# Kernel tuning notes

Hardware: AMD Instinct MI355X
Metric: run time of the kernel (lower is better)

## Reference

```python
import jax, jax.numpy as jnp
import numpy as np

D_MODEL = 512
D_ALPHA = 100
D_PH = 80
SCALE = 1.0 / np.sqrt(D_MODEL)


def gru_cell(x, h, Wih, Whh, bih, bhh):
    # PyTorch GRU gate order: r, z, n
    gi = x @ Wih.T + bih
    gh = h @ Whh.T + bhh
    ir, iz, inn = jnp.split(gi, 3, axis=-1)
    hr, hz, hn = jnp.split(gh, 3, axis=-1)
    r = jax.nn.sigmoid(ir + hr)
    z = jax.nn.sigmoid(iz + hz)
    n = jnp.tanh(inn + r * hn)
    return (1.0 - z) * n + z * h


def attend(q, k, v):
    # q: [B,D], k/v: [B,L,D]
    scores = jnp.einsum('bd,bld->bl', q, k) * SCALE
    a = jax.nn.softmax(scores, axis=-1)  # [B,L]
    o = jnp.einsum('bl,bld->bd', a, v)
    return a, o


def setup_inputs() -> dict:
    key = jax.random.key(0)
    ks = jax.random.split(key, 25)
    D = D_MODEL

    def u(k, shape, fan):
        return jax.random.uniform(k, shape, jnp.float32, -1.0, 1.0) / np.sqrt(fan)

    inp = {
        'text': jax.random.randint(ks[0], (256, 128), 0, D_ALPHA),
        'tgt': jax.random.randint(ks[1], (256, 64), 0, D_PH),
        'E_alpha': jax.random.normal(ks[2], (D_ALPHA, D), jnp.float32),
        'enc_Wih_f': u(ks[3], (3 * D, D), D),
        'enc_Whh_f': u(ks[4], (3 * D, D), D),
        'enc_bih_f': u(ks[5], (3 * D,), D),
        'enc_bhh_f': u(ks[6], (3 * D,), D),
        'enc_Wih_b': u(ks[7], (3 * D, D), D),
        'enc_Whh_b': u(ks[8], (3 * D, D), D),
        'enc_bih_b': u(ks[9], (3 * D,), D),
        'enc_bhh_b': u(ks[10], (3 * D,), D),
        'hpost_W': u(ks[11], (D, 2 * D), 2 * D),
        'hpost_b': u(ks[12], (D,), 2 * D),
        'wk_W': u(ks[13], (D, 2 * D), 2 * D),
        'wk_b': u(ks[14], (D,), 2 * D),
        'wv_W': u(ks[15], (D, 2 * D), 2 * D),
        'wv_b': u(ks[16], (D,), 2 * D),
        'E_ph': jax.random.normal(ks[17], (D_PH, D), jnp.float32),
        'dec_Wih': u(ks[18], (3 * D, 2 * D), 2 * D),
        'dec_Whh': u(ks[19], (3 * D, D), D),
        'dec_bih': u(ks[20], (3 * D,), D),
        'dec_bhh': u(ks[21], (3 * D,), D),
        'post_W': u(ks[22], (D_PH, D), D),
        'post_b': u(ks[23], (D_PH,), D),
    }
    return inp


def reference(text, tgt, E_alpha, enc_Wih_f, enc_Whh_f, enc_bih_f, enc_bhh_f,
              enc_Wih_b, enc_Whh_b, enc_bih_b, enc_bhh_b, hpost_W, hpost_b,
              wk_W, wk_b, wv_W, wv_b, E_ph, dec_Wih, dec_Whh, dec_bih,
              dec_bhh, post_W, post_b):
    B, LT = text.shape
    LP = tgt.shape[1]

    # ---- Encoder: bidirectional single-layer GRU (eval: dropout = identity)
    emb = E_alpha[text]                     # [B,LT,D]
    xs = jnp.swapaxes(emb, 0, 1)            # [LT,B,D]
    h0 = jnp.zeros((B, D_MODEL), emb.dtype)

    def mk_step(Wih, Whh, bih, bhh):
        def step(h, x):
            h2 = gru_cell(x, h, Wih, Whh, bih, bhh)
            return h2, h2
        return step

    hF, ysF = jax.lax.scan(mk_step(enc_Wih_f, enc_Whh_f, enc_bih_f, enc_bhh_f), h0, xs)
    hB, ysB = jax.lax.scan(mk_step(enc_Wih_b, enc_Whh_b, enc_bih_b, enc_bhh_b), h0, xs[::-1])
    ysB = ysB[::-1]
    enc_o = jnp.swapaxes(jnp.concatenate([ysF, ysB], axis=-1), 0, 1)  # [B,LT,2D]
    h = jnp.tanh(jnp.concatenate([hF, hB], axis=-1) @ hpost_W.T + hpost_b)  # [B,D]

    k = enc_o @ wk_W.T + wk_b               # [B,LT,D]
    v = enc_o @ wv_W.T + wv_b               # [B,LT,D]

    # ---- initial attention from encoder hidden; eval-mode first token is argmax
    # over tgt[:,0] reshaped to [B,1,1], i.e. always index 0.
    a_sl0, a_o0 = attend(h, k, v)
    dec_i0 = jnp.zeros((B,), jnp.int32)

    def dstep(carry, _):
        hh, a_o, a_sl, dec_i = carry
        e = E_ph[dec_i]                                  # [B,D]
        x = gru_cell(jnp.concatenate([e, a_o], axis=-1), hh,
                     dec_Wih, dec_Whh, dec_bih, dec_bhh)  # [B,D]
        o = x @ post_W.T + post_b                         # [B,D_PH]
        n_sl, n_o = attend(x, k, v)
        nxt = jnp.argmax(o, axis=-1).astype(jnp.int32)
        return (x, n_o, n_sl, nxt), (a_sl, o)

    _, (attn_t, res_t) = jax.lax.scan(dstep, (h, a_o0, a_sl0, dec_i0), None, length=LP)
    attn = jnp.swapaxes(attn_t, 0, 1)        # [B,LP,LT]
    res = jnp.swapaxes(res_t, 0, 1)          # [B,LP,D_PH]
    return attn, res
```

## Files before the change

kernel.cpp:

```cpp
#include <hip/hip_runtime.h>
#include <math.h>

#define B   256
#define LT  128
#define LP  64
#define DM  512
#define D3  1536
#define DPH 80
#define SCALE_F 0.044194173824159216f

__device__ __forceinline__ float dot4(float4 a, float4 b) {
    return a.x*b.x + a.y*b.y + a.z*b.z + a.w*b.w;
}
__device__ __forceinline__ float sigmoidf_(float x) {
    return 1.0f / (1.0f + expf(-x));
}

__device__ __forceinline__ float4 issue_bypass4(const float* p) {
    float4 v;
    asm volatile("global_load_dwordx4 %0, %1, off sc0 sc1"
                 : "=v"(v) : "v"(p));
    return v;
}
__device__ __forceinline__ void wait_vm0() {
    asm volatile("s_waitcnt vmcnt(0)" ::: "memory");
    __builtin_amdgcn_sched_barrier(0);
}

__device__ __forceinline__ void group_barrier(int* cnt, int target) {
    __syncthreads();
    if (threadIdx.x == 0) {
        __hip_atomic_fetch_add(cnt, 1, __ATOMIC_RELEASE,
                               __HIP_MEMORY_SCOPE_AGENT);
        while (__hip_atomic_load(cnt, __ATOMIC_RELAXED,
                                 __HIP_MEMORY_SCOPE_AGENT) < target)
            __builtin_amdgcn_s_sleep(16);
    }
    __syncthreads();
}

__global__ __launch_bounds__(256) void precompG_kernel(
    const float* __restrict__ Emb, const float* __restrict__ W,
    const float* __restrict__ bias, float* __restrict__ G,
    int wstride, int woff)
{
    const int n  = blockIdx.x * 256 + threadIdx.x;
    const int r0 = blockIdx.y * 4;
    __shared__ float es[4][DM];
    for (int i = threadIdx.x; i < 4 * DM; i += 256)
        es[i >> 9][i & 511] = Emb[(r0 + (i >> 9)) * DM + (i & 511)];
    __syncthreads();
    float acc[4] = {0.f, 0.f, 0.f, 0.f};
    const float* wr = &W[(size_t)n * wstride + woff];
    for (int j = 0; j < DM; j += 4) {
        float4 w4 = *(const float4*)&wr[j];
        #pragma unroll
        for (int rr = 0; rr < 4; ++rr) {
            float4 e4 = *(const float4*)&es[rr][j];
            acc[rr] += dot4(e4, w4);
        }
    }
    float bv = bias[n];
    #pragma unroll
    for (int rr = 0; rr < 4; ++rr)
        G[(r0 + rr) * D3 + n] = acc[rr] + bv;
}

__global__ __launch_bounds__(512, 1) void enc_persist_kernel(
    const float* __restrict__ Gf, const float* __restrict__ Gb,
    const float* __restrict__ Whh_f, const float* __restrict__ Whh_b,
    const float* __restrict__ bhh_f, const float* __restrict__ bhh_b,
    const int* __restrict__ text,
    float* __restrict__ hF0, float* __restrict__ hF1,
    float* __restrict__ hB0, float* __restrict__ hB1,
    float* __restrict__ E,
    const float* __restrict__ hpost_W, const float* __restrict__ hpost_b,
    float* __restrict__ hd0, int* __restrict__ bar)
{
    __shared__ float Wl[48][516];
    __shared__ float As[2][64][36];
    __shared__ float xs[1024];
    __shared__ float bl[48];

    const int tid  = threadIdx.x;
    const int blk  = blockIdx.x;
    const int dir  = blk & 1;
    const int bblk = (blk >> 1) & 3;
    const int jblk = blk >> 3;
    const int jtile = jblk * 16;
    const int btile = bblk * 64;
    int* cnt = bar + (blk & 7);

    const float* G   = dir ? Gb : Gf;
    const float* Whh = dir ? Whh_b : Whh_f;
    const float* bhh = dir ? bhh_b : bhh_f;
    float* h0 = dir ? hB0 : hF0;
    float* h1 = dir ? hB1 : hF1;
    const int yoff = dir ? DM : 0;

    for (int i = tid; i < 48 * 128; i += 512) {
        const int r = i >> 7, c = (i & 127) << 2;
        *(float4*)&Wl[r][c] =
            *(const float4*)&Whh[(size_t)((r >> 4) * DM + jtile + (r & 15)) * DM + c];
    }
    if (tid < 48) bl[tid] = bhh[(tid >> 4) * DM + jtile + (tid & 15)];
    __syncthreads();

    const int jj   = tid & 15;
    const int rg   = tid >> 4;
    const int lrow = tid >> 3;
    const int lcol = (tid & 7) * 4;

    for (int s = 0; s < LT; ++s) {
        const int t = dir ? (LT - 1 - s) : s;
        const float* hin = (s & 1) ? h1 : h0;
        float* hout      = (s & 1) ? h0 : h1;

        float acc[2][3];
        #pragma unroll
        for (int m = 0; m < 2; ++m) {
            acc[m][0] = 0.f; acc[m][1] = 0.f; acc[m][2] = 0.f;
        }

        float4 rA = issue_bypass4(&hin[(btile + lrow) * DM + lcol]);
        wait_vm0();
        int buf = 0;
        for (int kc = 0; kc < 16; ++kc) {
            *(float4*)&As[buf][lrow][lcol] = rA;
            __syncthreads();
            float4 nA;
            if (kc < 15)
                nA = issue_bypass4(&hin[(btile + lrow) * DM + (kc + 1) * 32 + lcol]);
            const int kb = kc * 32;
            #pragma unroll
            for (int c4 = 0; c4 < 8; ++c4) {
                float4 bv0 = *(float4*)&Wl[jj][kb + c4 * 4];
                float4 bv1 = *(float4*)&Wl[16 + jj][kb + c4 * 4];
                float4 bv2 = *(float4*)&Wl[32 + jj][kb + c4 * 4];
                #pragma unroll
                for (int m = 0; m < 2; ++m) {
                    float4 av = *(float4*)&As[buf][rg * 2 + m][c4 * 4];
                    acc[m][0] += dot4(av, bv0);
                    acc[m][1] += dot4(av, bv1);
                    acc[m][2] += dot4(av, bv2);
                }
            }
            if (kc < 15) { wait_vm0(); rA = nA; }
            buf ^= 1;
        }

        const int j = jtile + jj;
        #pragma unroll
        for (int m = 0; m < 2; ++m) {
            const int b = btile + rg * 2 + m;
            const int c = text[b * LT + t];
            float hr = acc[m][0] + bl[jj];
            float hz = acc[m][1] + bl[16 + jj];
            float hn = acc[m][2] + bl[32 + jj];
            float r = sigmoidf_(G[c * D3 + j] + hr);
            float z = sigmoidf_(G[c * D3 + DM + j] + hz);
            float n = tanhf(G[c * D3 + 2 * DM + j] + r * hn);
            float hp = hin[b * DM + j];
            float hv = (1.f - z) * n + z * hp;
            hout[b * DM + j] = hv;
            E[(size_t)(b * LT + t) * 1024 + yoff + j] = hv;
        }
        if (s < LT - 1) group_barrier(cnt, 32 * (s + 1));
    }

    group_barrier(bar + 8, 256);
    {
        const int b = blk;
        if (tid < 256) {
            float4 v = issue_bypass4((tid < 128)
                ? &hF0[b * DM + tid * 4]
                : &hB0[b * DM + (tid - 128) * 4]);
            wait_vm0();
            *(float4*)&xs[tid * 4] = v;
        }
        __syncthreads();
        if (tid < DM) {
            const float* wr = &hpost_W[tid * 1024];
            float acc = 0.f;
            for (int jx = 0; jx < 1024; jx += 4)
                acc += dot4(*(const float4*)&xs[jx], *(const float4*)&wr[jx]);
            hd0[b * DM + tid] = tanhf(acc + hpost_b[tid]);
        }
    }
}

__global__ __launch_bounds__(256) void kv_chunk_kernel(
    const float* __restrict__ E,
    const float* __restrict__ wk, const float* __restrict__ wv,
    const float* __restrict__ kb, const float* __restrict__ vb,
    float* __restrict__ T, int r0)
{
    __shared__ float As[64][36];
    __shared__ float Bk[64][36];
    __shared__ float Bv[64][36];
    const int tid = threadIdx.x;
    const int nn = tid & 15, bb = tid >> 4;
    const int ntile = blockIdx.x * 64;
    const int mtile = blockIdx.y * 64;

    float ak[4][4], av_[4][4];
    #pragma unroll
    for (int m = 0; m < 4; ++m)
        #pragma unroll
        for (int i = 0; i < 4; ++i) { ak[m][i] = 0.f; av_[m][i] = 0.f; }

    const int lrow = tid >> 3;
    const int lcol = (tid & 7) * 4;

    for (int k0 = 0; k0 < 1024; k0 += 32) {
        __syncthreads();
        *(float4*)&As[lrow][lcol] =
            *(const float4*)&E[(size_t)(r0 + mtile + lrow) * 1024 + k0 + lcol];
        *(float4*)&As[lrow + 32][lcol] =
            *(const float4*)&E[(size_t)(r0 + mtile + lrow + 32) * 1024 + k0 + lcol];
        *(float4*)&Bk[lrow][lcol] =
            *(const float4*)&wk[(ntile + lrow) * 1024 + k0 + lcol];
        *(float4*)&Bk[lrow + 32][lcol] =
            *(const float4*)&wk[(ntile + lrow + 32) * 1024 + k0 + lcol];
        *(float4*)&Bv[lrow][lcol] =
            *(const float4*)&wv[(ntile + lrow) * 1024 + k0 + lcol];
        *(float4*)&Bv[lrow + 32][lcol] =
            *(const float4*)&wv[(ntile + lrow + 32) * 1024 + k0 + lcol];
        __syncthreads();
        #pragma unroll
        for (int c4 = 0; c4 < 8; ++c4) {
            float4 a4[4], k4[4], v4[4];
            #pragma unroll
            for (int m = 0; m < 4; ++m) a4[m] = *(float4*)&As[bb + 16 * m][c4 * 4];
            #pragma unroll
            for (int i = 0; i < 4; ++i) {
                k4[i] = *(float4*)&Bk[nn + 16 * i][c4 * 4];
                v4[i] = *(float4*)&Bv[nn + 16 * i][c4 * 4];
            }
            #pragma unroll
            for (int m = 0; m < 4; ++m)
                #pragma unroll
                for (int i = 0; i < 4; ++i) {
                    ak[m][i]  += dot4(a4[m], k4[i]);
                    av_[m][i] += dot4(a4[m], v4[i]);
                }
        }
    }
    #pragma unroll
    for (int m = 0; m < 4; ++m) {
        const int lm = mtile + bb + 16 * m;
        #pragma unroll
        for (int i = 0; i < 4; ++i) {
            const int gn = ntile + nn + 16 * i;
            T[(size_t)lm * 1024 + gn]       = ak[m][i]  + kb[gn];
            T[(size_t)lm * 1024 + DM + gn]  = av_[m][i] + vb[gn];
        }
    }
}

__global__ __launch_bounds__(256) void copy4_kernel(
    float4* __restrict__ dst, const float4* __restrict__ src, int n4)
{
    int i = blockIdx.x * 256 + threadIdx.x;
    const int stride = gridDim.x * 256;
    for (; i < n4; i += stride) dst[i] = src[i];
}

__device__ __forceinline__ void attend_body(
    int b, int tid, const float* __restrict__ q, const float* __restrict__ EKV,
    const float* __restrict__ post_W, const float* __restrict__ post_b,
    float* __restrict__ attn, float* __restrict__ res,
    float* __restrict__ a_o, int* __restrict__ dec_i,
    int s, int attn_row, int do_post, int do_attn,
    float* qs, float* part, float* sarr, float* red, float4 (*pvp)[128])
{
    if (tid < 128) {
        float4 qv = issue_bypass4(&q[b * DM + tid * 4]);
        wait_vm0();
        *(float4*)&qs[tid * 4] = qv;
    }
    __syncthreads();

    if (do_post) {
        if (tid < DPH) {
            const float* wr = &post_W[tid * DM];
            float acc = 0.f;
            for (int d = 0; d < DM; d += 4)
                acc += dot4(*(const float4*)&qs[d], *(const float4*)&wr[d]);
            float lv = acc + post_b[tid];
            res[(size_t)(b * LP + s) * DPH + tid] = lv;
            part[tid] = lv;
        }
        __syncthreads();
        if (tid == 0) {
            float best = part[0]; int bi = 0;
            for (int p = 1; p < DPH; ++p) {
                float vv = part[p];
                if (vv > best) { best = vv; bi = p; }
            }
            dec_i[b] = bi;
        }
        __syncthreads();
    }

    if (do_attn) {
        {
            const int r = tid & 127, quad = tid >> 7;
            const float* kr = &EKV[(size_t)(b * LT + r) * 1024 + quad * 128];
            const float* qh = &qs[quad * 128];
            float p0 = 0.f, p1 = 0.f;
            #pragma unroll
            for (int d = 0; d < 128; d += 8) {
                p0 += dot4(*(const float4*)&qh[d],     *(const float4*)&kr[d]);
                p1 += dot4(*(const float4*)&qh[d + 4], *(const float4*)&kr[d + 4]);
            }
            part[tid] = p0 + p1;
        }
        __syncthreads();
        if (tid < LT)
            sarr[tid] = (((part[tid] + part[tid + 128]) + part[tid + 256])
                         + part[tid + 384]) * SCALE_F;
        __syncthreads();
        if (tid < 64) {
            float m = fmaxf(sarr[tid], sarr[tid + 64]);
            #pragma unroll
            for (int off = 32; off > 0; off >>= 1)
                m = fmaxf(m, __shfl_xor(m, off));
            if (tid == 0) red[0] = m;
        }
        __syncthreads();
        const float smax = red[0];
        if (tid < LT) sarr[tid] = expf(sarr[tid] - smax);
        __syncthreads();
        if (tid < 64) {
            float ssum = sarr[tid] + sarr[tid + 64];
            #pragma unroll
            for (int off = 32; off > 0; off >>= 1)
                ssum += __shfl_xor(ssum, off);
            if (tid == 0) red[1] = ssum;
        }
        __syncthreads();
        const float inv = 1.0f / red[1];
        if (tid < LT) {
            float a = sarr[tid] * inv;
            sarr[tid] = a;
            attn[(size_t)(b * LP + attn_row) * LT + tid] = a;
        }
        __syncthreads();
        {
            const int d4 = tid & 127, quad = tid >> 7;
            const float* vb0 = &EKV[(size_t)b * LT * 1024 + DM];
            float4 a0 = make_float4(0.f, 0.f, 0.f, 0.f);
            float4 a1 = make_float4(0.f, 0.f, 0.f, 0.f);
            const int l0 = quad * 32;
            #pragma unroll
            for (int l = l0; l < l0 + 32; l += 2) {
                float w0 = sarr[l], w1 = sarr[l + 1];
                float4 v0 = *(const float4*)&vb0[(size_t)l * 1024 + d4 * 4];
                float4 v1 = *(const float4*)&vb0[(size_t)(l + 1) * 1024 + d4 * 4];
                a0.x += w0 * v0.x; a0.y += w0 * v0.y;
                a0.z += w0 * v0.z; a0.w += w0 * v0.w;
                a1.x += w1 * v1.x; a1.y += w1 * v1.y;
                a1.z += w1 * v1.z; a1.w += w1 * v1.w;
            }
            pvp[quad][d4] = make_float4(a0.x + a1.x, a0.y + a1.y,
                                        a0.z + a1.z, a0.w + a1.w);
        }
        __syncthreads();
        if (tid < 128) {
            float4 p0 = pvp[0][tid], p1 = pvp[1][tid];
            float4 p2 = pvp[2][tid], p3 = pvp[3][tid];
            float4 o = make_float4(((p0.x + p1.x) + p2.x) + p3.x,
                                   ((p0.y + p1.y) + p2.y) + p3.y,
                                   ((p0.z + p1.z) + p2.z) + p3.z,
                                   ((p0.w + p1.w) + p2.w) + p3.w);
            *(float4*)&a_o[b * DM + tid * 4] = o;
        }
    }
}

__global__ __launch_bounds__(512, 1) void dec_persist_kernel(
    const float* __restrict__ Gd,
    const float* __restrict__ dec_Wih, const float* __restrict__ dec_Whh,
    const float* __restrict__ dec_bhh,
    const float* __restrict__ EKV,
    const float* __restrict__ post_W, const float* __restrict__ post_b,
    float* __restrict__ attn, float* __restrict__ res,
    float* __restrict__ a_o, int* __restrict__ dec_i,
    float* __restrict__ hd0, float* __restrict__ hd1,
    int* __restrict__ bar)
{
    __shared__ float Wi[24][516];
    __shared__ float Wh[24][516];
    __shared__ float As[2][64][36];
    __shared__ float bl[24];
    __shared__ float qs[DM];
    __shared__ float part[512];
    __shared__ float sarr[LT];
    __shared__ float red[2];
    __shared__ float4 pvp[4][128];

    const int tid  = threadIdx.x;
    const int blk  = blockIdx.x;
    const int bblk = blk & 3;
    const int jblk = blk >> 2;
    const int jtile = jblk * 8;
    const int btile = bblk * 64;
    const int arow  = btile + jblk;
    int* cnt = bar + 9 + bblk;
    int nb = 0;

    for (int i = tid; i < 24 * 128; i += 512) {
        const int r = i >> 7, c = (i & 127) << 2;
        const int wrow = (r >> 3) * DM + jtile + (r & 7);
        *(float4*)&Wi[r][c] =
            *(const float4*)&dec_Wih[(size_t)wrow * 1024 + DM + c];
        *(float4*)&Wh[r][c] =
            *(const float4*)&dec_Whh[(size_t)wrow * DM + c];
    }
    if (tid < 24) bl[tid] = dec_bhh[(tid >> 3) * DM + jtile + (tid & 7)];
    __syncthreads();

    attend_body(arow, tid, hd0, EKV, post_W, post_b, attn, res, a_o, dec_i,
                0, 0, 0, 1, qs, part, sarr, red, pvp);
    ++nb; group_barrier(cnt, 64 * nb);

    const int jj   = tid & 7;
    const int rr   = tid >> 3;
    const int lrow = tid >> 3;
    const int lcol = (tid & 7) * 4;

    for (int s = 0; s < LP; ++s) {
        const float* hin = (s & 1) ? hd1 : hd0;
        float* hout      = (s & 1) ? hd0 : hd1;

        float acc[4] = {0.f, 0.f, 0.f, 0.f};

        #pragma unroll
        for (int ph = 0; ph < 2; ++ph) {
            const float* Aptr = (ph == 0) ? a_o : hin;
            const float (*W)[516] = (ph == 0) ? Wi : Wh;

            float4 rA = issue_bypass4(&Aptr[(btile + lrow) * DM + lcol]);
            wait_vm0();
            int buf = (ph == 0) ? 0 : 0;
            for (int kc = 0; kc < 16; ++kc) {
                *(float4*)&As[buf][lrow][lcol] = rA;
                __syncthreads();
                float4 nA;
                if (kc < 15)
                    nA = issue_bypass4(&Aptr[(btile + lrow) * DM + (kc + 1) * 32 + lcol]);
                const int kb = kc * 32;
                #pragma unroll
                for (int c4 = 0; c4 < 8; ++c4) {
                    float4 bv0 = *(float4*)&W[jj][kb + c4 * 4];
                    float4 bv1 = *(float4*)&W[8 + jj][kb + c4 * 4];
                    float4 bv2 = *(float4*)&W[16 + jj][kb + c4 * 4];
                    float4 av  = *(float4*)&As[buf][rr][c4 * 4];
                    acc[0]      += dot4(av, bv0);
                    acc[1]      += dot4(av, bv1);
                    acc[2 + ph] += dot4(av, bv2);
                }
                if (kc < 15) { wait_vm0(); rA = nA; }
                buf ^= 1;
            }
            __syncthreads();
        }

        {
            const int j = jtile + jj;
            const int b = btile + rr;
            const int c = __hip_atomic_load(&dec_i[b], __ATOMIC_RELAXED,
                                            __HIP_MEMORY_SCOPE_SYSTEM);
            float r = sigmoidf_(Gd[c * D3 + j] + bl[jj] + acc[0]);
            float z = sigmoidf_(Gd[c * D3 + DM + j] + bl[8 + jj] + acc[1]);
            float n = tanhf(Gd[c * D3 + 2 * DM + j] + acc[2]
                            + r * (acc[3] + bl[16 + jj]));
            float hp = hin[b * DM + j];
            hout[b * DM + j] = (1.f - z) * n + z * hp;
        }
        ++nb; group_barrier(cnt, 64 * nb);

        attend_body(arow, tid, hout, EKV, post_W, post_b, attn, res, a_o, dec_i,
                    s, s + 1, 1, (s < LP - 1) ? 1 : 0,
                    qs, part, sarr, red, pvp);
        if (s < LP - 1) { ++nb; group_barrier(cnt, 64 * nb); }
    }
}

extern "C" void kernel_launch(void* const* d_in, const int* in_sizes, int n_in,
                              void* d_out, int out_size, void* d_ws, size_t ws_size,
                              hipStream_t stream)
{
    const int*   text    = (const int*)d_in[0];
    const float* E_alpha = (const float*)d_in[2];
    const float* Wih_f   = (const float*)d_in[3];
    const float* Whh_f   = (const float*)d_in[4];
    const float* bih_f   = (const float*)d_in[5];
    const float* bhh_f   = (const float*)d_in[6];
    const float* Wih_b   = (const float*)d_in[7];
    const float* Whh_b   = (const float*)d_in[8];
    const float* bih_b   = (const float*)d_in[9];
    const float* bhh_b   = (const float*)d_in[10];
    const float* hpost_W = (const float*)d_in[11];
    const float* hpost_b = (const float*)d_in[12];
    const float* wk_W    = (const float*)d_in[13];
    const float* wk_b    = (const float*)d_in[14];
    const float* wv_W    = (const float*)d_in[15];
    const float* wv_b    = (const float*)d_in[16];
    const float* E_ph    = (const float*)d_in[17];
    const float* dec_Wih = (const float*)d_in[18];
    const float* dec_Whh = (const float*)d_in[19];
    const float* dec_bih = (const float*)d_in[20];
    const float* dec_bhh = (const float*)d_in[21];
    const float* post_W  = (const float*)d_in[22];
    const float* post_b  = (const float*)d_in[23];

    float* ws = (float*)d_ws;
    float* Gf  = ws;
    float* Gb  = Gf  + 153600;
    float* Gd  = Gb  + 153600;
    float* hF0 = Gd  + 122880;
    float* hF1 = hF0 + 131072;
    float* hB0 = hF1 + 131072;
    float* hB1 = hB0 + 131072;
    float* hd0 = hB1 + 131072;
    float* hd1 = hd0 + 131072;
    float* a_o = hd1 + 131072;
    int*   dec_i = (int*)(a_o + 131072);
    int*   bar   = dec_i + 256;
    float* E   = a_o + 131072 + 512;
    float* T   = E + 33554432;

    hipMemsetAsync(hF0, 0, 131072 * sizeof(float), stream);
    hipMemsetAsync(hB0, 0, 131072 * sizeof(float), stream);
    hipMemsetAsync(dec_i, 0, (256 + 16) * sizeof(int), stream);

    precompG_kernel<<<dim3(6, 25), 256, 0, stream>>>(E_alpha, Wih_f, bih_f, Gf, DM, 0);
    precompG_kernel<<<dim3(6, 25), 256, 0, stream>>>(E_alpha, Wih_b, bih_b, Gb, DM, 0);
    precompG_kernel<<<dim3(6, 20), 256, 0, stream>>>(E_ph, dec_Wih, dec_bih, Gd, 1024, 0);

    enc_persist_kernel<<<dim3(256), 512, 0, stream>>>(
        Gf, Gb, Whh_f, Whh_b, bhh_f, bhh_b, text,
        hF0, hF1, hB0, hB1, E, hpost_W, hpost_b, hd0, bar);

    for (int c = 0; c < 2; ++c) {
        const int r0 = c * 16384;
        kv_chunk_kernel<<<dim3(8, 256), 256, 0, stream>>>(
            E, wk_W, wv_W, wk_b, wv_b, T, r0);
        copy4_kernel<<<dim3(4096), 256, 0, stream>>>(
            (float4*)(E + (size_t)r0 * 1024), (const float4*)T,
            16384 * 1024 / 4);
    }

    float* attn = (float*)d_out;
    float* res  = attn + (size_t)B * LP * LT;

    dec_persist_kernel<<<dim3(256), 512, 0, stream>>>(
        Gd, dec_Wih, dec_Whh, dec_bhh, E, post_W, post_b,
        attn, res, a_o, dec_i, hd0, hd1, bar);
}
```

Before: 12.03 ms.

## Stream transposed recurrent weights from global, prefetch gate inputs, enlarge KV tile

Adds a transpose kernel that lays out the recurrent GRU weights as k4-major float4 arrays. The encoder and decoder persistent kernels now read these weights straight from global/L2 each step instead of staging them in LDS, which frees a large LDS footprint. Gate precomputations and previous hidden values are now loaded before the matmul loop, so their latency overlaps with it. The KV projection tile grows from 64 to 128 rows, and the barrier spin sleep is shortened. The risk is that repeated global weight reads every timestep add memory traffic and latency where LDS reads were cheap.

```diff
diff --git a/kernel.cpp b/kernel.cpp
--- a/kernel.cpp
+++ b/kernel.cpp
@@ -34,9 +34,21 @@
                                __HIP_MEMORY_SCOPE_AGENT);
         while (__hip_atomic_load(cnt, __ATOMIC_RELAXED,
                                  __HIP_MEMORY_SCOPE_AGENT) < target)
-            __builtin_amdgcn_s_sleep(16);
+            __builtin_amdgcn_s_sleep(8);
     }
     __syncthreads();
+}
+
+__global__ __launch_bounds__(256) void transW_kernel(
+    const float* __restrict__ W, float4* __restrict__ Wt,
+    int wstride, int woff)
+{
+    const int idx = blockIdx.x * 256 + threadIdx.x;
+    const int j   = idx & 511;
+    const int k4  = (idx >> 9) & 127;
+    const int g   = idx >> 16;
+    const float* src = &W[(size_t)(g * 512 + j) * wstride + woff + k4 * 4];
+    Wt[idx] = make_float4(src[0], src[1], src[2], src[3]);
 }
 
 __global__ __launch_bounds__(256) void precompG_kernel(
@@ -68,7 +80,7 @@
 
 __global__ __launch_bounds__(512, 1) void enc_persist_kernel(
     const float* __restrict__ Gf, const float* __restrict__ Gb,
-    const float* __restrict__ Whh_f, const float* __restrict__ Whh_b,
+    const float4* __restrict__ WtF, const float4* __restrict__ WtB,
     const float* __restrict__ bhh_f, const float* __restrict__ bhh_b,
     const int* __restrict__ text,
     float* __restrict__ hF0, float* __restrict__ hF1,
@@ -77,7 +89,6 @@
     const float* __restrict__ hpost_W, const float* __restrict__ hpost_b,
     float* __restrict__ hd0, int* __restrict__ bar)
 {
-    __shared__ float Wl[48][516];
     __shared__ float As[2][64][36];
     __shared__ float xs[1024];
     __shared__ float bl[48];
@@ -91,18 +102,13 @@
     const int btile = bblk * 64;
     int* cnt = bar + (blk & 7);
 
-    const float* G   = dir ? Gb : Gf;
-    const float* Whh = dir ? Whh_b : Whh_f;
-    const float* bhh = dir ? bhh_b : bhh_f;
+    const float* G    = dir ? Gb : Gf;
+    const float4* Wt  = dir ? WtB : WtF;
+    const float* bhh  = dir ? bhh_b : bhh_f;
     float* h0 = dir ? hB0 : hF0;
     float* h1 = dir ? hB1 : hF1;
     const int yoff = dir ? DM : 0;
 
-    for (int i = tid; i < 48 * 128; i += 512) {
-        const int r = i >> 7, c = (i & 127) << 2;
-        *(float4*)&Wl[r][c] =
-            *(const float4*)&Whh[(size_t)((r >> 4) * DM + jtile + (r & 15)) * DM + c];
-    }
     if (tid < 48) bl[tid] = bhh[(tid >> 4) * DM + jtile + (tid & 15)];
     __syncthreads();
 
@@ -110,11 +116,26 @@
     const int rg   = tid >> 4;
     const int lrow = tid >> 3;
     const int lcol = (tid & 7) * 4;
+    const int j    = jtile + jj;
+    const float4* w0 = Wt + j;
+    const float4* w1 = Wt + 128 * 512 + j;
+    const float4* w2 = Wt + 256 * 512 + j;
 
     for (int s = 0; s < LT; ++s) {
         const int t = dir ? (LT - 1 - s) : s;
         const float* hin = (s & 1) ? h1 : h0;
         float* hout      = (s & 1) ? h0 : h1;
+
+        float pg[2][3], php[2];
+        #pragma unroll
+        for (int m = 0; m < 2; ++m) {
+            const int b = btile + rg * 2 + m;
+            const int c = text[b * LT + t];
+            pg[m][0] = G[c * D3 + j];
+            pg[m][1] = G[c * D3 + DM + j];
+            pg[m][2] = G[c * D3 + 2 * DM + j];
+            php[m]   = hin[b * DM + j];
+        }
 
         float acc[2][3];
         #pragma unroll
@@ -131,12 +152,12 @@
             float4 nA;
             if (kc < 15)
                 nA = issue_bypass4(&hin[(btile + lrow) * DM + (kc + 1) * 32 + lcol]);
-            const int kb = kc * 32;
             #pragma unroll
             for (int c4 = 0; c4 < 8; ++c4) {
-                float4 bv0 = *(float4*)&Wl[jj][kb + c4 * 4];
-                float4 bv1 = *(float4*)&Wl[16 + jj][kb + c4 * 4];
-                float4 bv2 = *(float4*)&Wl[32 + jj][kb + c4 * 4];
+                const int k4 = kc * 8 + c4;
+                float4 bv0 = w0[k4 * 512];
+                float4 bv1 = w1[k4 * 512];
+                float4 bv2 = w2[k4 * 512];
                 #pragma unroll
                 for (int m = 0; m < 2; ++m) {
                     float4 av = *(float4*)&As[buf][rg * 2 + m][c4 * 4];
@@ -149,19 +170,16 @@
             buf ^= 1;
         }
 
-        const int j = jtile + jj;
         #pragma unroll
         for (int m = 0; m < 2; ++m) {
             const int b = btile + rg * 2 + m;
-            const int c = text[b * LT + t];
             float hr = acc[m][0] + bl[jj];
             float hz = acc[m][1] + bl[16 + jj];
             float hn = acc[m][2] + bl[32 + jj];
-            float r = sigmoidf_(G[c * D3 + j] + hr);
-            float z = sigmoidf_(G[c * D3 + DM + j] + hz);
-            float n = tanhf(G[c * D3 + 2 * DM + j] + r * hn);
-            float hp = hin[b * DM + j];
-            float hv = (1.f - z) * n + z * hp;
+            float r = sigmoidf_(pg[m][0] + hr);
+            float z = sigmoidf_(pg[m][1] + hz);
+            float n = tanhf(pg[m][2] + r * hn);
+            float hv = (1.f - z) * n + z * php[m];
             hout[b * DM + j] = hv;
             E[(size_t)(b * LT + t) * 1024 + yoff + j] = hv;
         }
@@ -195,17 +213,17 @@
     const float* __restrict__ kb, const float* __restrict__ vb,
     float* __restrict__ T, int r0)
 {
-    __shared__ float As[64][36];
+    __shared__ float As[128][36];
     __shared__ float Bk[64][36];
     __shared__ float Bv[64][36];
     const int tid = threadIdx.x;
     const int nn = tid & 15, bb = tid >> 4;
     const int ntile = blockIdx.x * 64;
-    const int mtile = blockIdx.y * 64;
-
-    float ak[4][4], av_[4][4];
+    const int mtile = blockIdx.y * 128;
+
+    float ak[8][4], av_[8][4];
     #pragma unroll
-    for (int m = 0; m < 4; ++m)
+    for (int m = 0; m < 8; ++m)
         #pragma unroll
         for (int i = 0; i < 4; ++i) { ak[m][i] = 0.f; av_[m][i] = 0.f; }
 
@@ -214,10 +232,10 @@
 
     for (int k0 = 0; k0 < 1024; k0 += 32) {
         __syncthreads();
-        *(float4*)&As[lrow][lcol] =
-            *(const float4*)&E[(size_t)(r0 + mtile + lrow) * 1024 + k0 + lcol];
-        *(float4*)&As[lrow + 32][lcol] =
-            *(const float4*)&E[(size_t)(r0 + mtile + lrow + 32) * 1024 + k0 + lcol];
+        #pragma unroll
+        for (int q = 0; q < 4; ++q)
+            *(float4*)&As[lrow + 32 * q][lcol] =
+                *(const float4*)&E[(size_t)(r0 + mtile + lrow + 32 * q) * 1024 + k0 + lcol];
         *(float4*)&Bk[lrow][lcol] =
             *(const float4*)&wk[(ntile + lrow) * 1024 + k0 + lcol];
         *(float4*)&Bk[lrow + 32][lcol] =
@@ -229,16 +247,16 @@
         __syncthreads();
         #pragma unroll
         for (int c4 = 0; c4 < 8; ++c4) {
-            float4 a4[4], k4[4], v4[4];
-            #pragma unroll
-            for (int m = 0; m < 4; ++m) a4[m] = *(float4*)&As[bb + 16 * m][c4 * 4];
+            float4 a4[8], k4[4], v4[4];
+            #pragma unroll
+            for (int m = 0; m < 8; ++m) a4[m] = *(float4*)&As[bb + 16 * m][c4 * 4];
             #pragma unroll
             for (int i = 0; i < 4; ++i) {
                 k4[i] = *(float4*)&Bk[nn + 16 * i][c4 * 4];
                 v4[i] = *(float4*)&Bv[nn + 16 * i][c4 * 4];
             }
             #pragma unroll
-            for (int m = 0; m < 4; ++m)
+            for (int m = 0; m < 8; ++m)
                 #pragma unroll
                 for (int i = 0; i < 4; ++i) {
                     ak[m][i]  += dot4(a4[m], k4[i]);
@@ -247,7 +265,7 @@
         }
     }
     #pragma unroll
-    for (int m = 0; m < 4; ++m) {
+    for (int m = 0; m < 8; ++m) {
         const int lm = mtile + bb + 16 * m;
         #pragma unroll
         for (int i = 0; i < 4; ++i) {
@@ -381,7 +399,7 @@
 
 __global__ __launch_bounds__(512, 1) void dec_persist_kernel(
     const float* __restrict__ Gd,
-    const float* __restrict__ dec_Wih, const float* __restrict__ dec_Whh,
+    const float4* __restrict__ WtI, const float4* __restrict__ WtH,
     const float* __restrict__ dec_bhh,
     const float* __restrict__ EKV,
     const float* __restrict__ post_W, const float* __restrict__ post_b,
@@ -390,8 +408,6 @@
     float* __restrict__ hd0, float* __restrict__ hd1,
     int* __restrict__ bar)
 {
-    __shared__ float Wi[24][516];
-    __shared__ float Wh[24][516];
     __shared__ float As[2][64][36];
     __shared__ float bl[24];
     __shared__ float qs[DM];
@@ -410,14 +426,6 @@
     int* cnt = bar + 9 + bblk;
     int nb = 0;
 
-    for (int i = tid; i < 24 * 128; i += 512) {
-        const int r = i >> 7, c = (i & 127) << 2;
-        const int wrow = (r >> 3) * DM + jtile + (r & 7);
-        *(float4*)&Wi[r][c] =
-            *(const float4*)&dec_Wih[(size_t)wrow * 1024 + DM + c];
-        *(float4*)&Wh[r][c] =
-            *(const float4*)&dec_Whh[(size_t)wrow * DM + c];
-    }
     if (tid < 24) bl[tid] = dec_bhh[(tid >> 3) * DM + jtile + (tid & 7)];
     __syncthreads();
 
@@ -429,33 +437,45 @@
     const int rr   = tid >> 3;
     const int lrow = tid >> 3;
     const int lcol = (tid & 7) * 4;
+    const int j    = jtile + jj;
+    const int b_   = btile + rr;
 
     for (int s = 0; s < LP; ++s) {
         const float* hin = (s & 1) ? hd1 : hd0;
         float* hout      = (s & 1) ? hd0 : hd1;
 
+        const int c_ = __hip_atomic_load(&dec_i[b_], __ATOMIC_RELAXED,
+                                         __HIP_MEMORY_SCOPE_SYSTEM);
+        const float pg0 = Gd[c_ * D3 + j];
+        const float pg1 = Gd[c_ * D3 + DM + j];
+        const float pg2 = Gd[c_ * D3 + 2 * DM + j];
+        const float php_ = hin[b_ * DM + j];
+
         float acc[4] = {0.f, 0.f, 0.f, 0.f};
 
         #pragma unroll
         for (int ph = 0; ph < 2; ++ph) {
             const float* Aptr = (ph == 0) ? a_o : hin;
-            const float (*W)[516] = (ph == 0) ? Wi : Wh;
+            const float4* Wt  = (ph == 0) ? WtI : WtH;
+            const float4* w0 = Wt + j;
+            const float4* w1 = Wt + 128 * 512 + j;
+            const float4* w2 = Wt + 256 * 512 + j;
 
             float4 rA = issue_bypass4(&Aptr[(btile + lrow) * DM + lcol]);
             wait_vm0();
-            int buf = (ph == 0) ? 0 : 0;
+            int buf = 0;
             for (int kc = 0; kc < 16; ++kc) {
                 *(float4*)&As[buf][lrow][lcol] = rA;
                 __syncthreads();
                 float4 nA;
                 if (kc < 15)
                     nA = issue_bypass4(&Aptr[(btile + lrow) * DM + (kc + 1) * 32 + lcol]);
-                const int kb = kc * 32;
                 #pragma unroll
                 for (int c4 = 0; c4 < 8; ++c4) {
-                    float4 bv0 = *(float4*)&W[jj][kb + c4 * 4];
-                    float4 bv1 = *(float4*)&W[8 + jj][kb + c4 * 4];
-                    float4 bv2 = *(float4*)&W[16 + jj][kb + c4 * 4];
+                    const int k4 = kc * 8 + c4;
+                    float4 bv0 = w0[k4 * 512];
+                    float4 bv1 = w1[k4 * 512];
+                    float4 bv2 = w2[k4 * 512];
                     float4 av  = *(float4*)&As[buf][rr][c4 * 4];
                     acc[0]      += dot4(av, bv0);
                     acc[1]      += dot4(av, bv1);
@@ -468,16 +488,10 @@
         }
 
         {
-            const int j = jtile + jj;
-            const int b = btile + rr;
-            const int c = __hip_atomic_load(&dec_i[b], __ATOMIC_RELAXED,
-                                            __HIP_MEMORY_SCOPE_SYSTEM);
-            float r = sigmoidf_(Gd[c * D3 + j] + bl[jj] + acc[0]);
-            float z = sigmoidf_(Gd[c * D3 + DM + j] + bl[8 + jj] + acc[1]);
-            float n = tanhf(Gd[c * D3 + 2 * DM + j] + acc[2]
-                            + r * (acc[3] + bl[16 + jj]));
-            float hp = hin[b * DM + j];
-            hout[b * DM + j] = (1.f - z) * n + z * hp;
+            float r = sigmoidf_(pg0 + bl[jj] + acc[0]);
+            float z = sigmoidf_(pg1 + bl[8 + jj] + acc[1]);
+            float n = tanhf(pg2 + acc[2] + r * (acc[3] + bl[16 + jj]));
+            hout[b_ * DM + j] = (1.f - z) * n + z * php_;
         }
         ++nb; group_barrier(cnt, 64 * nb);
 
@@ -529,24 +543,33 @@
     float* a_o = hd1 + 131072;
     int*   dec_i = (int*)(a_o + 131072);
     int*   bar   = dec_i + 256;
-    float* E   = a_o + 131072 + 512;
+    float* WtF = a_o + 131072 + 512;
+    float* WtB = WtF + 786432;
+    float* WtI = WtB + 786432;
+    float* WtH = WtI + 786432;
+    float* E   = WtH + 786432;
     float* T   = E + 33554432;
 
     hipMemsetAsync(hF0, 0, 131072 * sizeof(float), stream);
     hipMemsetAsync(hB0, 0, 131072 * sizeof(float), stream);
     hipMemsetAsync(dec_i, 0, (256 + 16) * sizeof(int), stream);
 
+    transW_kernel<<<dim3(768), 256, 0, stream>>>(Whh_f, (float4*)WtF, DM, 0);
+    transW_kernel<<<dim3(768), 256, 0, stream>>>(Whh_b, (float4*)WtB, DM, 0);
+    transW_kernel<<<dim3(768), 256, 0, stream>>>(dec_Wih, (float4*)WtI, 1024, DM);
+    transW_kernel<<<dim3(768), 256, 0, stream>>>(dec_Whh, (float4*)WtH, DM, 0);
+
     precompG_kernel<<<dim3(6, 25), 256, 0, stream>>>(E_alpha, Wih_f, bih_f, Gf, DM, 0);
     precompG_kernel<<<dim3(6, 25), 256, 0, stream>>>(E_alpha, Wih_b, bih_b, Gb, DM, 0);
     precompG_kernel<<<dim3(6, 20), 256, 0, stream>>>(E_ph, dec_Wih, dec_bih, Gd, 1024, 0);
 
     enc_persist_kernel<<<dim3(256), 512, 0, stream>>>(
-        Gf, Gb, Whh_f, Whh_b, bhh_f, bhh_b, text,
+        Gf, Gb, (const float4*)WtF, (const float4*)WtB, bhh_f, bhh_b, text,
         hF0, hF1, hB0, hB1, E, hpost_W, hpost_b, hd0, bar);
 
     for (int c = 0; c < 2; ++c) {
         const int r0 = c * 16384;
-        kv_chunk_kernel<<<dim3(8, 256), 256, 0, stream>>>(
+        kv_chunk_kernel<<<dim3(8, 128), 256, 0, stream>>>(
             E, wk_W, wv_W, wk_b, wv_b, T, r0);
         copy4_kernel<<<dim3(4096), 256, 0, stream>>>(
             (float4*)(E + (size_t)r0 * 1024), (const float4*)T,
@@ -557,6 +580,6 @@
     float* res  = attn + (size_t)B * LP * LT;
 
     dec_persist_kernel<<<dim3(256), 512, 0, stream>>>(
-        Gd, dec_Wih, dec_Whh, dec_bhh, E, post_W, post_b,
+        Gd, (const float4*)WtI, (const float4*)WtH, dec_bhh, E, post_W, post_b,
         attn, res, a_o, dec_i, hd0, hd1, bar);
 }
```

Result: slower. 26.76 ms (+122.4%).
